# Kernel tuning notes

Hardware: AMD Instinct MI355X
Metric: run time of the kernel (lower is better)

Reference implementation:

```python
import jax, jax.numpy as jnp
import numpy as np

T = 3072          # num tokens
HID = 5120        # hidden_size
H = 16            # num_local_heads
DN = 128          # qk_nope_head_dim
DR = 64           # qk_rope_head_dim
DQK = DN + DR     # qk_head_dim = 192
DV = 128          # v_head_dim
Q_RANK = 1536     # q_lora_rank
KV_RANK = 512     # kv_lora_rank


def rmsnorm(x, w, eps=1e-6):
    var = jnp.mean(jnp.square(x), axis=-1, keepdims=True)
    return x * jax.lax.rsqrt(var + eps) * w


def apply_rope(x, cos, sin):
    # neox-style rotate-half; x [..., DR], cos/sin broadcastable [..., DR//2]
    x1, x2 = jnp.split(x, 2, axis=-1)
    return jnp.concatenate([x1 * cos - x2 * sin, x2 * cos + x1 * sin], axis=-1)


def setup_inputs() -> dict:
    key = jax.random.key(0)
    ks = jax.random.split(key, 8)
    s = 0.02
    positions = jnp.arange(T, dtype=jnp.int32)
    hidden_states = jax.random.normal(ks[0], (T, HID), dtype=jnp.float32)
    llama_4_scaling = jnp.ones((T, 1, 1), dtype=jnp.float32)
    w_q_a = jax.random.normal(ks[1], (HID, Q_RANK), dtype=jnp.float32) * s
    q_a_ln_w = jnp.ones((Q_RANK,), dtype=jnp.float32)
    w_q_b = jax.random.normal(ks[2], (Q_RANK, H * DQK), dtype=jnp.float32) * s
    w_kv_a = jax.random.normal(ks[3], (HID, KV_RANK + DR), dtype=jnp.float32) * s
    kv_a_ln_w = jnp.ones((KV_RANK,), dtype=jnp.float32)
    w_kv_b = jax.random.normal(ks[4], (KV_RANK, H * (DN + DV)), dtype=jnp.float32) * s
    w_o = jax.random.normal(ks[5], (H * DV, HID), dtype=jnp.float32) * s
    # cos/sin cache: [max_pos, DR]; first half cos, second half sin
    inv_freq = 1.0 / (10000.0 ** (jnp.arange(0, DR, 2, dtype=jnp.float32) / DR))
    t = jnp.arange(T, dtype=jnp.float32)
    freqs = t[:, None] * inv_freq[None, :]              # [T, DR//2]
    cos_sin_cache = jnp.concatenate([jnp.cos(freqs), jnp.sin(freqs)], axis=-1)
    return {
        "positions": positions, "hidden_states": hidden_states,
        "llama_4_scaling": llama_4_scaling,
        "w_q_a": w_q_a, "q_a_ln_w": q_a_ln_w, "w_q_b": w_q_b,
        "w_kv_a": w_kv_a, "kv_a_ln_w": kv_a_ln_w, "w_kv_b": w_kv_b,
        "w_o": w_o, "cos_sin_cache": cos_sin_cache,
    }


def reference(positions, hidden_states, llama_4_scaling, w_q_a, q_a_ln_w,
              w_q_b, w_kv_a, kv_a_ln_w, w_kv_b, w_o, cos_sin_cache):
    # ---- Q path: low-rank down/up projection with RMSNorm ----
    q = rmsnorm(hidden_states @ w_q_a, q_a_ln_w) @ w_q_b       # [T, H*DQK]
    q = q.reshape(T, H, DQK)
    q_nope, q_pe = q[..., :DN], q[..., DN:]                    # [T,H,DN],[T,H,DR]

    # ---- KV path: compressed latent + shared rope key ----
    latent = hidden_states @ w_kv_a                            # [T, KV_RANK+DR]
    kv_a = rmsnorm(latent[:, :KV_RANK], kv_a_ln_w)             # [T, KV_RANK]
    k_pe = latent[:, KV_RANK:]                                 # [T, DR] (shared across heads)
    kv = (kv_a @ w_kv_b).reshape(T, H, DN + DV)
    k_nope, v = kv[..., :DN], kv[..., DN:]                     # [T,H,DN],[T,H,DV]

    # ---- partial RoPE on the rope slices only ----
    cs = cos_sin_cache[positions]                              # [T, DR]
    cos, sin = cs[:, :DR // 2], cs[:, DR // 2:]
    q_pe = apply_rope(q_pe, cos[:, None, :], sin[:, None, :])
    k_pe = apply_rope(k_pe, cos, sin)

    q = jnp.concatenate([q_nope, q_pe], axis=-1)               # [T, H, DQK]
    k = jnp.concatenate(
        [k_nope, jnp.broadcast_to(k_pe[:, None, :], (T, H, DR))], axis=-1)

    q = q * llama_4_scaling

    # ---- causal attention (v is zero-padded to DQK in the original;
    #      the pad contributes zeros and is sliced off, so we skip it) ----
    scale = 1.0 / jnp.sqrt(jnp.float32(DQK))
    scores = jnp.einsum('qhd,khd->hqk', q, k) * scale          # [H, T, T]
    causal = positions[:, None] >= positions[None, :]
    scores = jnp.where(causal[None, :, :], scores, jnp.finfo(scores.dtype).min)
    probs = jax.nn.softmax(scores, axis=-1)
    attn = jnp.einsum('hqk,khd->qhd', probs, v)                # [T, H, DV]

    return attn.reshape(T, H * DV) @ w_o                       # [T, HID]
```

## Files before the change

kernel.cpp:

```cpp
#include <hip/hip_runtime.h>
#include <hip/hip_bf16.h>
#include <math.h>

#define T_TOK 3072
#define HID_D 5120
#define NH 16
#define DN 128
#define DR 64
#define DQK 192
#define DV 128
#define QRANK 1536
#define KVRANK 512
#define MERGED_N 2176

typedef __attribute__((ext_vector_type(8))) short short8;
typedef __attribute__((ext_vector_type(4))) float f32x4;
typedef unsigned short u16;

__device__ __forceinline__ u16 f2bf(float f) {
    unsigned int u = __float_as_uint(f);
    unsigned int lsb = (u >> 16) & 1;
    u += 0x7fffu + lsb;
    return (u16)(u >> 16);
}
__device__ __forceinline__ float bf2f(u16 v) {
    return __uint_as_float(((unsigned int)v) << 16);
}

__device__ __forceinline__ void gload_lds16(const u16* g, u16* l) {
    __builtin_amdgcn_global_load_lds((const __attribute__((address_space(1))) void*)g,
                                     (__attribute__((address_space(3))) void*)l, 16, 0, 0);
}

__global__ __launch_bounds__(256) void convert_bf_k(const float* __restrict__ x,
                                                    u16* __restrict__ y, int n4)
{
    const int i = blockIdx.x * 256 + threadIdx.x;
    if (i < n4) {
        float4 v = ((const float4*)x)[i];
        ushort4 o;
        o.x = f2bf(v.x); o.y = f2bf(v.y); o.z = f2bf(v.z); o.w = f2bf(v.w);
        ((ushort4*)y)[i] = o;
    }
}

__global__ __launch_bounds__(256) void transpose_conv_k(const float* __restrict__ W,
                                                        u16* __restrict__ WT,
                                                        int K, int N)
{
    __shared__ float tile[32][33];
    const int n0 = blockIdx.x * 32, k0 = blockIdx.y * 32;
    const int tx = threadIdx.x & 31, ty = threadIdx.x >> 5;
#pragma unroll
    for (int i = 0; i < 32; i += 8) {
        const int nn = n0 + tx;
        tile[ty + i][tx] = (nn < N) ? W[(size_t)(k0 + ty + i) * N + nn] : 0.f;
    }
    __syncthreads();
#pragma unroll
    for (int i = 0; i < 32; i += 8) {
        WT[(size_t)(n0 + ty + i) * K + k0 + tx] = f2bf(tile[tx][ty + i]);
    }
}

template <bool BF16_OUT>
__global__ __launch_bounds__(256) void bgemm_bt_k(
    const u16* __restrict__ A, const u16* __restrict__ BT, void* __restrict__ C,
    int Nreal, int K, int lda, int ldb, int ldc)
{
    __shared__ __attribute__((aligned(16))) u16 As[128 * 32];
    __shared__ __attribute__((aligned(16))) u16 Bs[128 * 32];

    const int tid  = threadIdx.x;
    const int wave = tid >> 6, lane = tid & 63;
    const int quad = lane >> 4, l16 = lane & 15;
    const int wr = (wave >> 1) * 64, wc = (wave & 1) * 64;
    const int row0 = blockIdx.y * 128, col0 = blockIdx.x * 128;

    f32x4 acc[4][4];
#pragma unroll
    for (int i = 0; i < 4; ++i)
#pragma unroll
        for (int j = 0; j < 4; ++j) acc[i][j] = (f32x4){0.f, 0.f, 0.f, 0.f};

    const int sr  = tid >> 2;
    const int skc = (tid & 3) * 8;
    const u16* ap0 = A  + (size_t)(row0 + sr)      * lda + skc;
    const u16* ap1 = A  + (size_t)(row0 + sr + 64) * lda + skc;
    const u16* bp0 = BT + (size_t)(col0 + sr)      * ldb + skc;
    const u16* bp1 = BT + (size_t)(col0 + sr + 64) * ldb + skc;
    u16* al0 = As + tid * 8;
    u16* al1 = As + tid * 8 + 64 * 32;
    u16* bl0 = Bs + tid * 8;
    u16* bl1 = Bs + tid * 8 + 64 * 32;

    for (int kt = 0; kt < K; kt += 32) {
        gload_lds16(ap0 + kt, al0);
        gload_lds16(ap1 + kt, al1);
        gload_lds16(bp0 + kt, bl0);
        gload_lds16(bp1 + kt, bl1);
        __syncthreads();

        short8 af[4], bf[4];
#pragma unroll
        for (int mi = 0; mi < 4; ++mi)
            af[mi] = *(const short8*)(As + (wr + mi * 16 + l16) * 32 + quad * 8);
#pragma unroll
        for (int ni = 0; ni < 4; ++ni)
            bf[ni] = *(const short8*)(Bs + (wc + ni * 16 + l16) * 32 + quad * 8);
#pragma unroll
        for (int mi = 0; mi < 4; ++mi)
#pragma unroll
            for (int ni = 0; ni < 4; ++ni)
                acc[mi][ni] = __builtin_amdgcn_mfma_f32_16x16x32_bf16(
                    af[mi], bf[ni], acc[mi][ni], 0, 0, 0);
        __syncthreads();
    }

#pragma unroll
    for (int mi = 0; mi < 4; ++mi) {
#pragma unroll
        for (int ni = 0; ni < 4; ++ni) {
            const int col_g = col0 + wc + ni * 16 + l16;
            if (col_g < Nreal) {
#pragma unroll
                for (int r = 0; r < 4; ++r) {
                    const int row_g = row0 + wr + mi * 16 + quad * 4 + r;
                    if (BF16_OUT)
                        ((u16*)C)[(size_t)row_g * ldc + col_g] = f2bf(acc[mi][ni][r]);
                    else
                        ((float*)C)[(size_t)row_g * ldc + col_g] = acc[mi][ni][r];
                }
            }
        }
    }
}

__global__ __launch_bounds__(256) void rmsnorm_bf_k(const u16* __restrict__ x,
                                                    const float* __restrict__ w,
                                                    u16* __restrict__ y,
                                                    int width, int stride, int off)
{
    const int row = blockIdx.x;
    const u16* xr = x + (size_t)row * stride + off;
    const int nch = width >> 3;
    float ss = 0.f;
    for (int i = threadIdx.x; i < nch; i += 256) {
        short8 v = *(const short8*)(xr + i * 8);
#pragma unroll
        for (int j = 0; j < 8; ++j) { const float f = bf2f((u16)v[j]); ss += f * f; }
    }
    __shared__ float red[256];
    red[threadIdx.x] = ss;
    __syncthreads();
    for (int s2 = 128; s2 > 0; s2 >>= 1) {
        if (threadIdx.x < s2) red[threadIdx.x] += red[threadIdx.x + s2];
        __syncthreads();
    }
    const float scale = rsqrtf(red[0] / (float)width + 1e-6f);
    u16* yr = y + (size_t)row * width;
    for (int i = threadIdx.x; i < nch; i += 256) {
        short8 v = *(const short8*)(xr + i * 8);
        const float4 w0 = *(const float4*)(w + i * 8);
        const float4 w1 = *(const float4*)(w + i * 8 + 4);
        short8 o;
        o[0] = (short)f2bf(bf2f((u16)v[0]) * scale * w0.x);
        o[1] = (short)f2bf(bf2f((u16)v[1]) * scale * w0.y);
        o[2] = (short)f2bf(bf2f((u16)v[2]) * scale * w0.z);
        o[3] = (short)f2bf(bf2f((u16)v[3]) * scale * w0.w);
        o[4] = (short)f2bf(bf2f((u16)v[4]) * scale * w1.x);
        o[5] = (short)f2bf(bf2f((u16)v[5]) * scale * w1.y);
        o[6] = (short)f2bf(bf2f((u16)v[6]) * scale * w1.z);
        o[7] = (short)f2bf(bf2f((u16)v[7]) * scale * w1.w);
        *(short8*)(yr + i * 8) = o;
    }
}

__global__ __launch_bounds__(256) void rope_scale_q_bf_k(const u16* __restrict__ q, const int* __restrict__ positions,
                                  const float* __restrict__ scaling,
                                  const float* __restrict__ cs_cache, u16* __restrict__ qb)
{
    const int t = blockIdx.x;
    const int pos = positions[t];
    const float* cs = cs_cache + (size_t)pos * DR;
    const float s = scaling[t];
    __shared__ float c_sh[32], s_sh[32];
    if (threadIdx.x < 32) {
        c_sh[threadIdx.x] = cs[threadIdx.x];
        s_sh[threadIdx.x] = cs[32 + threadIdx.x];
    }
    __syncthreads();
    const u16* qt = q + (size_t)t * NH * DQK;
    u16* qo = qb + (size_t)t * NH * DQK;
    for (int cc = threadIdx.x; cc < NH * 20; cc += 256) {
        const int hh = cc / 20, c = cc % 20;
        const u16* qr = qt + hh * DQK;
        u16* qw = qo + hh * DQK;
        if (c < 16) {
            short8 v = *(const short8*)(qr + c * 8);
            short8 o;
#pragma unroll
            for (int j = 0; j < 8; ++j) o[j] = (short)f2bf(bf2f((u16)v[j]) * s);
            *(short8*)(qw + c * 8) = o;
        } else {
            const int d0 = (c - 16) * 8;
            short8 x1 = *(const short8*)(qr + 128 + d0);
            short8 x2 = *(const short8*)(qr + 160 + d0);
            short8 o1, o2;
#pragma unroll
            for (int j = 0; j < 8; ++j) {
                const float a = bf2f((u16)x1[j]), b = bf2f((u16)x2[j]);
                const float cv = c_sh[d0 + j], sv = s_sh[d0 + j];
                o1[j] = (short)f2bf((a * cv - b * sv) * s);
                o2[j] = (short)f2bf((b * cv + a * sv) * s);
            }
            *(short8*)(qw + 128 + d0) = o1;
            *(short8*)(qw + 160 + d0) = o2;
        }
    }
}

__global__ void rope_k_bf_k(const u16* __restrict__ qa_lat, u16* __restrict__ kpe,
                            const int* __restrict__ positions,
                            const float* __restrict__ cs_cache)
{
    const int t = blockIdx.x;
    const int d = threadIdx.x;
    if (d >= 32) return;
    const int pos = positions[t];
    const float* cs = cs_cache + (size_t)pos * DR;
    const float c = cs[d], sn = cs[32 + d];
    const u16* lr = qa_lat + (size_t)t * MERGED_N + QRANK + KVRANK;
    const float x1 = bf2f(lr[d]), x2 = bf2f(lr[32 + d]);
    kpe[(size_t)t * DR + d]      = f2bf(x1 * c - x2 * sn);
    kpe[(size_t)t * DR + 32 + d] = f2bf(x2 * c + x1 * sn);
}

__global__ __launch_bounds__(256) void transpose_v_k(const u16* __restrict__ kvb,
                                                     u16* __restrict__ vt)
{
    __shared__ u16 tile[64][72];
    const int t0 = blockIdx.x * 64, d0 = blockIdx.y * 64, h = blockIdx.z;
    const int tid = threadIdx.x;
    for (int cc = tid; cc < 64 * 8; cc += 256) {
        const int row = cc >> 3, c = (cc & 7) * 8;
        *(short8*)&tile[row][c] =
            *(const short8*)(kvb + ((size_t)(t0 + row) * NH + h) * (DN + DV) + DN + d0 + c);
    }
    __syncthreads();
    for (int cc = tid; cc < 64 * 8; cc += 256) {
        const int drow = cc >> 3, c = (cc & 7) * 8;
        short8 s;
#pragma unroll
        for (int j = 0; j < 8; ++j) s[j] = tile[c + j][drow];
        *(short8*)(vt + ((size_t)h * DV + d0 + drow) * T_TOK + t0 + c) = s;
    }
}

#define ATT_BM 128
#define ATT_BN 64
__global__ __launch_bounds__(512, 4) void attn_mfma_k(
    const u16* __restrict__ qb, const u16* __restrict__ kvb,
    const u16* __restrict__ kpeb, const u16* __restrict__ vt,
    u16* __restrict__ attnb)
{
    __shared__ u16 Ks[ATT_BN][200];
    __shared__ u16 Vt[DV][72];
    __shared__ u16 Ps[8][16][72];

    const int tid  = threadIdx.x;
    const int wave = tid >> 6;
    const int lane = tid & 63;
    const int quad = lane >> 4;
    const int l16  = lane & 15;

    const int bid   = (int)blockIdx.x;
    const int chunk = bid & 7;
    const int local = bid >> 3;
    const int h     = chunk * 2 + (local & 1);
    const int qblk  = (T_TOK / ATT_BM - 1) - (local >> 1);
    const int q0    = qblk * ATT_BM;
    const int wrow0 = q0 + wave * 16;
    const int qrow  = wrow0 + l16;

    short8 qf[6];
    {
        const u16* qp = qb + ((size_t)qrow * NH + h) * DQK + quad * 8;
#pragma unroll
        for (int c = 0; c < 6; ++c)
            qf[c] = *(const short8*)(qp + c * 32);
    }

    const u16* gp[5];
    size_t     gst[5];
    u16*       ld[5];
#pragma unroll
    for (int i = 0; i < 3; ++i) {
        const int cc = tid + 512 * i;
        const int row = cc / 24, c = cc % 24;
        if (c < 16) {
            gp[i]  = kvb + ((size_t)row * NH + h) * (DN + DV) + c * 8;
            gst[i] = (size_t)ATT_BN * NH * (DN + DV);
        } else {
            gp[i]  = kpeb + (size_t)row * DR + (c - 16) * 8;
            gst[i] = (size_t)ATT_BN * DR;
        }
        ld[i] = &Ks[row][c * 8];
    }
#pragma unroll
    for (int i = 0; i < 2; ++i) {
        const int cc = tid + 512 * i;
        const int row = cc >> 3, c = (cc & 7) * 8;
        gp[3 + i]  = vt + ((size_t)h * DV + row) * T_TOK + c;
        gst[3 + i] = (size_t)ATT_BN;
        ld[3 + i]  = &Vt[row][c];
    }

    f32x4 oacc[8];
#pragma unroll
    for (int t = 0; t < 8; ++t) oacc[t] = (f32x4){0.f, 0.f, 0.f, 0.f};
    float m_old[4], l_run[4];
#pragma unroll
    for (int r = 0; r < 4; ++r) { m_old[r] = -1e30f; l_run[r] = 0.f; }

    short8 streg[5];
#pragma unroll
    for (int i = 0; i < 5; ++i) streg[i] = *(const short8*)gp[i];

    const int nkt = (q0 + ATT_BM) / ATT_BN;
    for (int kt = 0; kt < nkt; ++kt) {
        __syncthreads();
#pragma unroll
        for (int i = 0; i < 5; ++i) *(short8*)ld[i] = streg[i];
        __syncthreads();
        if (kt + 1 < nkt) {
#pragma unroll
            for (int i = 0; i < 5; ++i)
                streg[i] = *(const short8*)(gp[i] + (size_t)(kt + 1) * gst[i]);
        }

        const int k0 = kt * ATT_BN;
        if (k0 <= wrow0 + 15) {
            f32x4 sacc[4];
#pragma unroll
            for (int t = 0; t < 4; ++t) sacc[t] = (f32x4){0.f, 0.f, 0.f, 0.f};
#pragma unroll
            for (int t = 0; t < 4; ++t) {
                const u16* kp = &Ks[t * 16 + l16][quad * 8];
#pragma unroll
                for (int c = 0; c < 6; ++c) {
                    short8 bfrag = *(const short8*)(kp + c * 32);
                    sacc[t] = __builtin_amdgcn_mfma_f32_16x16x32_bf16(qf[c], bfrag, sacc[t], 0, 0, 0);
                }
            }
            const float sc = 0.07216878364870322f;
            const int rbase = wrow0 + quad * 4;
            if (k0 + ATT_BN - 1 > wrow0) {
#pragma unroll
                for (int t = 0; t < 4; ++t) {
                    const int colg = k0 + t * 16 + l16;
#pragma unroll
                    for (int r = 0; r < 4; ++r) {
                        const float s = sacc[t][r] * sc;
                        sacc[t][r] = (rbase + r >= colg) ? s : -1e30f;
                    }
                }
            } else {
#pragma unroll
                for (int t = 0; t < 4; ++t)
#pragma unroll
                    for (int r = 0; r < 4; ++r) sacc[t][r] *= sc;
            }
            float alpha[4];
#pragma unroll
            for (int r = 0; r < 4; ++r) {
                float mx = fmaxf(fmaxf(sacc[0][r], sacc[1][r]), fmaxf(sacc[2][r], sacc[3][r]));
                mx = fmaxf(mx, __shfl_xor(mx, 1));
                mx = fmaxf(mx, __shfl_xor(mx, 2));
                mx = fmaxf(mx, __shfl_xor(mx, 4));
                mx = fmaxf(mx, __shfl_xor(mx, 8));
                const float mnew = fmaxf(m_old[r], mx);
                alpha[r] = __expf(m_old[r] - mnew);
                float sum = 0.f;
#pragma unroll
                for (int t = 0; t < 4; ++t) {
                    const float p = __expf(sacc[t][r] - mnew);
                    sacc[t][r] = p;
                    sum += p;
                }
                sum += __shfl_xor(sum, 1);
                sum += __shfl_xor(sum, 2);
                sum += __shfl_xor(sum, 4);
                sum += __shfl_xor(sum, 8);
                l_run[r] = l_run[r] * alpha[r] + sum;
                m_old[r] = mnew;
            }
#pragma unroll
            for (int t = 0; t < 4; ++t)
#pragma unroll
                for (int r = 0; r < 4; ++r)
                    Ps[wave][quad * 4 + r][t * 16 + l16] = f2bf(sacc[t][r]);
#pragma unroll
            for (int t = 0; t < 8; ++t)
#pragma unroll
                for (int r = 0; r < 4; ++r)
                    oacc[t][r] *= alpha[r];
#pragma unroll
            for (int ch = 0; ch < 2; ++ch) {
                short8 pfrag = *(const short8*)&Ps[wave][l16][ch * 32 + quad * 8];
#pragma unroll
                for (int t = 0; t < 8; ++t) {
                    short8 vfrag = *(const short8*)&Vt[t * 16 + l16][ch * 32 + quad * 8];
                    oacc[t] = __builtin_amdgcn_mfma_f32_16x16x32_bf16(pfrag, vfrag, oacc[t], 0, 0, 0);
                }
            }
        }
    }

#pragma unroll
    for (int r = 0; r < 4; ++r) {
        const float linv = 1.f / l_run[r];
        const int row_g = wrow0 + quad * 4 + r;
        u16* op = attnb + (size_t)row_g * (NH * DV) + h * DV;
#pragma unroll
        for (int t = 0; t < 8; ++t)
            op[t * 16 + l16] = f2bf(oacc[t][r] * linv);
    }
}

extern "C" void kernel_launch(void* const* d_in, const int* in_sizes, int n_in,
                              void* d_out, int out_size, void* d_ws, size_t ws_size,
                              hipStream_t stream)
{
    const int*   positions = (const int*)d_in[0];
    const float* hidden    = (const float*)d_in[1];
    const float* scaling   = (const float*)d_in[2];
    const float* w_q_a     = (const float*)d_in[3];
    const float* q_a_ln_w  = (const float*)d_in[4];
    const float* w_q_b     = (const float*)d_in[5];
    const float* w_kv_a    = (const float*)d_in[6];
    const float* kv_a_ln_w = (const float*)d_in[7];
    const float* w_kv_b    = (const float*)d_in[8];
    const float* w_o       = (const float*)d_in[9];
    const float* cs_cache  = (const float*)d_in[10];
    float* out = (float*)d_out;

    char* p = (char*)d_ws;
    auto alloc = [&](size_t bytes) { char* r = p; p += (bytes + 255) & ~(size_t)255; return r; };

    char* regH      = alloc((size_t)T_TOK * HID_D * 2);
    u16*  hidden_bf = (u16*)regH;
    u16*  qraw_bf   = (u16*)regH;
    char* regQ      = alloc((size_t)T_TOK * MERGED_N * 2 + (size_t)T_TOK * QRANK * 2);
    u16*  qa_lat    = (u16*)regQ;
    u16*  q_a_norm  = (u16*)(regQ + (size_t)T_TOK * MERGED_N * 2);
    u16*  qb        = (u16*)regQ;
    u16* kv_a_norm = (u16*)alloc((size_t)T_TOK * KVRANK * 2);
    u16* kpe_bf    = (u16*)alloc((size_t)T_TOK * DR * 2);
    u16* kv_bf     = (u16*)alloc((size_t)T_TOK * NH * (DN + DV) * 2);
    u16* vt        = (u16*)alloc((size_t)NH * DV * T_TOK * 2);
    u16* attnb     = (u16*)alloc((size_t)T_TOK * NH * DV * 2);
    u16* wqakva_bt = (u16*)alloc((size_t)MERGED_N * HID_D * 2);
    u16* wqb_bt    = (u16*)alloc((size_t)(NH * DQK) * QRANK * 2);
    u16* wkvb_bt   = (u16*)alloc((size_t)(NH * (DN + DV)) * KVRANK * 2);
    u16* wo_bt     = (u16*)alloc((size_t)HID_D * (NH * DV) * 2);

    const dim3 blk(256);

    convert_bf_k<<<dim3((T_TOK * HID_D / 4 + 255) / 256), blk, 0, stream>>>(
        hidden, hidden_bf, T_TOK * HID_D / 4);
    transpose_conv_k<<<dim3(QRANK / 32, HID_D / 32), blk, 0, stream>>>(
        w_q_a, wqakva_bt, HID_D, QRANK);
    transpose_conv_k<<<dim3(640 / 32, HID_D / 32), blk, 0, stream>>>(
        w_kv_a, wqakva_bt + (size_t)QRANK * HID_D, HID_D, KVRANK + DR);
    transpose_conv_k<<<dim3(NH * DQK / 32, QRANK / 32), blk, 0, stream>>>(w_q_b, wqb_bt, QRANK, NH * DQK);
    transpose_conv_k<<<dim3(NH * (DN + DV) / 32, KVRANK / 32), blk, 0, stream>>>(w_kv_b, wkvb_bt, KVRANK, NH * (DN + DV));
    transpose_conv_k<<<dim3(HID_D / 32, NH * DV / 32), blk, 0, stream>>>(w_o, wo_bt, NH * DV, HID_D);

    bgemm_bt_k<true><<<dim3(MERGED_N / 128, T_TOK / 128), blk, 0, stream>>>(
        hidden_bf, wqakva_bt, qa_lat, QRANK + KVRANK + DR, HID_D, HID_D, HID_D, MERGED_N);
    rope_k_bf_k<<<dim3(T_TOK), dim3(64), 0, stream>>>(qa_lat, kpe_bf, positions, cs_cache);
    rmsnorm_bf_k<<<dim3(T_TOK), blk, 0, stream>>>(qa_lat, q_a_ln_w, q_a_norm, QRANK, MERGED_N, 0);
    rmsnorm_bf_k<<<dim3(T_TOK), blk, 0, stream>>>(qa_lat, kv_a_ln_w, kv_a_norm, KVRANK, MERGED_N, QRANK);
    bgemm_bt_k<true><<<dim3(NH * DQK / 128, T_TOK / 128), blk, 0, stream>>>(
        q_a_norm, wqb_bt, qraw_bf, NH * DQK, QRANK, QRANK, QRANK, NH * DQK);
    rope_scale_q_bf_k<<<dim3(T_TOK), blk, 0, stream>>>(qraw_bf, positions, scaling, cs_cache, qb);
    bgemm_bt_k<true><<<dim3(NH * (DN + DV) / 128, T_TOK / 128), blk, 0, stream>>>(
        kv_a_norm, wkvb_bt, kv_bf, NH * (DN + DV), KVRANK, KVRANK, KVRANK, NH * (DN + DV));
    transpose_v_k<<<dim3(T_TOK / 64, DV / 64, NH), blk, 0, stream>>>(kv_bf, vt);
    attn_mfma_k<<<dim3(T_TOK / ATT_BM * NH), dim3(512), 0, stream>>>(qb, kv_bf, kpe_bf, vt, attnb);
    bgemm_bt_k<false><<<dim3(HID_D / 128, T_TOK / 128), blk, 0, stream>>>(
        attnb, wo_bt, out, HID_D, NH * DV, NH * DV, NH * DV, HID_D);
}
```

Measured before the change: 838.3 us.

## Load K and V fragments directly from global memory in attention, dropping LDS staging

The attention kernel no longer stages K/K_pe and transposed V tiles through shared memory with register prefetch and block barriers. Each wave now reads its MFMA B-operand fragments straight from global memory, with no __syncthreads in the key loop. Blocks shrink to 256 threads (4 waves, 64 query rows), the grid becomes 768 blocks, and each wave iterates only up to its own causal limit. This removes barrier and LDS traffic, but each wave reloads K/V independently, which increases global/L2 traffic and exposes load latency without explicit prefetch.

```diff
diff --git a/kernel.cpp b/kernel.cpp
--- a/kernel.cpp
+++ b/kernel.cpp
@@ -257,16 +257,12 @@
     }
 }
 
-#define ATT_BM 128
-#define ATT_BN 64
-__global__ __launch_bounds__(512, 4) void attn_mfma_k(
+__global__ __launch_bounds__(256) void attn_mfma_k(
     const u16* __restrict__ qb, const u16* __restrict__ kvb,
     const u16* __restrict__ kpeb, const u16* __restrict__ vt,
     u16* __restrict__ attnb)
 {
-    __shared__ u16 Ks[ATT_BN][200];
-    __shared__ u16 Vt[DV][72];
-    __shared__ u16 Ps[8][16][72];
+    __shared__ u16 Ps[4][16][72];
 
     const int tid  = threadIdx.x;
     const int wave = tid >> 6;
@@ -278,9 +274,8 @@
     const int chunk = bid & 7;
     const int local = bid >> 3;
     const int h     = chunk * 2 + (local & 1);
-    const int qblk  = (T_TOK / ATT_BM - 1) - (local >> 1);
-    const int q0    = qblk * ATT_BM;
-    const int wrow0 = q0 + wave * 16;
+    const int qb64  = 47 - (local >> 1);
+    const int wrow0 = qb64 * 64 + wave * 16;
     const int qrow  = wrow0 + l16;
 
     short8 qf[6];
@@ -291,31 +286,6 @@
             qf[c] = *(const short8*)(qp + c * 32);
     }
 
-    const u16* gp[5];
-    size_t     gst[5];
-    u16*       ld[5];
-#pragma unroll
-    for (int i = 0; i < 3; ++i) {
-        const int cc = tid + 512 * i;
-        const int row = cc / 24, c = cc % 24;
-        if (c < 16) {
-            gp[i]  = kvb + ((size_t)row * NH + h) * (DN + DV) + c * 8;
-            gst[i] = (size_t)ATT_BN * NH * (DN + DV);
-        } else {
-            gp[i]  = kpeb + (size_t)row * DR + (c - 16) * 8;
-            gst[i] = (size_t)ATT_BN * DR;
-        }
-        ld[i] = &Ks[row][c * 8];
-    }
-#pragma unroll
-    for (int i = 0; i < 2; ++i) {
-        const int cc = tid + 512 * i;
-        const int row = cc >> 3, c = (cc & 7) * 8;
-        gp[3 + i]  = vt + ((size_t)h * DV + row) * T_TOK + c;
-        gst[3 + i] = (size_t)ATT_BN;
-        ld[3 + i]  = &Vt[row][c];
-    }
-
     f32x4 oacc[8];
 #pragma unroll
     for (int t = 0; t < 8; ++t) oacc[t] = (f32x4){0.f, 0.f, 0.f, 0.f};
@@ -323,96 +293,91 @@
 #pragma unroll
     for (int r = 0; r < 4; ++r) { m_old[r] = -1e30f; l_run[r] = 0.f; }
 
-    short8 streg[5];
-#pragma unroll
-    for (int i = 0; i < 5; ++i) streg[i] = *(const short8*)gp[i];
-
-    const int nkt = (q0 + ATT_BM) / ATT_BN;
+    const u16* vbase = vt + ((size_t)h * DV + l16) * T_TOK + quad * 8;
+    const int nkt = wrow0 / 64 + 1;
+
     for (int kt = 0; kt < nkt; ++kt) {
-        __syncthreads();
-#pragma unroll
-        for (int i = 0; i < 5; ++i) *(short8*)ld[i] = streg[i];
-        __syncthreads();
-        if (kt + 1 < nkt) {
-#pragma unroll
-            for (int i = 0; i < 5; ++i)
-                streg[i] = *(const short8*)(gp[i] + (size_t)(kt + 1) * gst[i]);
-        }
-
-        const int k0 = kt * ATT_BN;
-        if (k0 <= wrow0 + 15) {
-            f32x4 sacc[4];
-#pragma unroll
-            for (int t = 0; t < 4; ++t) sacc[t] = (f32x4){0.f, 0.f, 0.f, 0.f};
+        const int k0 = kt * 64;
+        f32x4 sacc[4];
+#pragma unroll
+        for (int t = 0; t < 4; ++t) sacc[t] = (f32x4){0.f, 0.f, 0.f, 0.f};
+#pragma unroll
+        for (int t = 0; t < 4; ++t) {
+            const int krow = k0 + t * 16 + l16;
+            const u16* kr = kvb + ((size_t)krow * NH + h) * (DN + DV) + quad * 8;
+            const u16* pr = kpeb + (size_t)krow * DR + quad * 8;
+            short8 b0 = *(const short8*)(kr);
+            short8 b1 = *(const short8*)(kr + 32);
+            short8 b2 = *(const short8*)(kr + 64);
+            short8 b3 = *(const short8*)(kr + 96);
+            short8 b4 = *(const short8*)(pr);
+            short8 b5 = *(const short8*)(pr + 32);
+            sacc[t] = __builtin_amdgcn_mfma_f32_16x16x32_bf16(qf[0], b0, sacc[t], 0, 0, 0);
+            sacc[t] = __builtin_amdgcn_mfma_f32_16x16x32_bf16(qf[1], b1, sacc[t], 0, 0, 0);
+            sacc[t] = __builtin_amdgcn_mfma_f32_16x16x32_bf16(qf[2], b2, sacc[t], 0, 0, 0);
+            sacc[t] = __builtin_amdgcn_mfma_f32_16x16x32_bf16(qf[3], b3, sacc[t], 0, 0, 0);
+            sacc[t] = __builtin_amdgcn_mfma_f32_16x16x32_bf16(qf[4], b4, sacc[t], 0, 0, 0);
+            sacc[t] = __builtin_amdgcn_mfma_f32_16x16x32_bf16(qf[5], b5, sacc[t], 0, 0, 0);
+        }
+        const float sc = 0.07216878364870322f;
+        const int rbase = wrow0 + quad * 4;
+        if (kt == nkt - 1) {
 #pragma unroll
             for (int t = 0; t < 4; ++t) {
-                const u16* kp = &Ks[t * 16 + l16][quad * 8];
-#pragma unroll
-                for (int c = 0; c < 6; ++c) {
-                    short8 bfrag = *(const short8*)(kp + c * 32);
-                    sacc[t] = __builtin_amdgcn_mfma_f32_16x16x32_bf16(qf[c], bfrag, sacc[t], 0, 0, 0);
+                const int colg = k0 + t * 16 + l16;
+#pragma unroll
+                for (int r = 0; r < 4; ++r) {
+                    const float s = sacc[t][r] * sc;
+                    sacc[t][r] = (rbase + r >= colg) ? s : -1e30f;
                 }
             }
-            const float sc = 0.07216878364870322f;
-            const int rbase = wrow0 + quad * 4;
-            if (k0 + ATT_BN - 1 > wrow0) {
-#pragma unroll
-                for (int t = 0; t < 4; ++t) {
-                    const int colg = k0 + t * 16 + l16;
-#pragma unroll
-                    for (int r = 0; r < 4; ++r) {
-                        const float s = sacc[t][r] * sc;
-                        sacc[t][r] = (rbase + r >= colg) ? s : -1e30f;
-                    }
-                }
-            } else {
-#pragma unroll
-                for (int t = 0; t < 4; ++t)
-#pragma unroll
-                    for (int r = 0; r < 4; ++r) sacc[t][r] *= sc;
+        } else {
+#pragma unroll
+            for (int t = 0; t < 4; ++t)
+#pragma unroll
+                for (int r = 0; r < 4; ++r) sacc[t][r] *= sc;
+        }
+        float alpha[4];
+#pragma unroll
+        for (int r = 0; r < 4; ++r) {
+            float mx = fmaxf(fmaxf(sacc[0][r], sacc[1][r]), fmaxf(sacc[2][r], sacc[3][r]));
+            mx = fmaxf(mx, __shfl_xor(mx, 1));
+            mx = fmaxf(mx, __shfl_xor(mx, 2));
+            mx = fmaxf(mx, __shfl_xor(mx, 4));
+            mx = fmaxf(mx, __shfl_xor(mx, 8));
+            const float mnew = fmaxf(m_old[r], mx);
+            alpha[r] = __expf(m_old[r] - mnew);
+            float sum = 0.f;
+#pragma unroll
+            for (int t = 0; t < 4; ++t) {
+                const float p = __expf(sacc[t][r] - mnew);
+                sacc[t][r] = p;
+                sum += p;
             }
-            float alpha[4];
-#pragma unroll
-            for (int r = 0; r < 4; ++r) {
-                float mx = fmaxf(fmaxf(sacc[0][r], sacc[1][r]), fmaxf(sacc[2][r], sacc[3][r]));
-                mx = fmaxf(mx, __shfl_xor(mx, 1));
-                mx = fmaxf(mx, __shfl_xor(mx, 2));
-                mx = fmaxf(mx, __shfl_xor(mx, 4));
-                mx = fmaxf(mx, __shfl_xor(mx, 8));
-                const float mnew = fmaxf(m_old[r], mx);
-                alpha[r] = __expf(m_old[r] - mnew);
-                float sum = 0.f;
-#pragma unroll
-                for (int t = 0; t < 4; ++t) {
-                    const float p = __expf(sacc[t][r] - mnew);
-                    sacc[t][r] = p;
-                    sum += p;
-                }
-                sum += __shfl_xor(sum, 1);
-                sum += __shfl_xor(sum, 2);
-                sum += __shfl_xor(sum, 4);
-                sum += __shfl_xor(sum, 8);
-                l_run[r] = l_run[r] * alpha[r] + sum;
-                m_old[r] = mnew;
-            }
-#pragma unroll
-            for (int t = 0; t < 4; ++t)
-#pragma unroll
-                for (int r = 0; r < 4; ++r)
-                    Ps[wave][quad * 4 + r][t * 16 + l16] = f2bf(sacc[t][r]);
-#pragma unroll
-            for (int t = 0; t < 8; ++t)
-#pragma unroll
-                for (int r = 0; r < 4; ++r)
-                    oacc[t][r] *= alpha[r];
-#pragma unroll
-            for (int ch = 0; ch < 2; ++ch) {
-                short8 pfrag = *(const short8*)&Ps[wave][l16][ch * 32 + quad * 8];
-#pragma unroll
-                for (int t = 0; t < 8; ++t) {
-                    short8 vfrag = *(const short8*)&Vt[t * 16 + l16][ch * 32 + quad * 8];
-                    oacc[t] = __builtin_amdgcn_mfma_f32_16x16x32_bf16(pfrag, vfrag, oacc[t], 0, 0, 0);
-                }
+            sum += __shfl_xor(sum, 1);
+            sum += __shfl_xor(sum, 2);
+            sum += __shfl_xor(sum, 4);
+            sum += __shfl_xor(sum, 8);
+            l_run[r] = l_run[r] * alpha[r] + sum;
+            m_old[r] = mnew;
+        }
+#pragma unroll
+        for (int t = 0; t < 4; ++t)
+#pragma unroll
+            for (int r = 0; r < 4; ++r)
+                Ps[wave][quad * 4 + r][t * 16 + l16] = f2bf(sacc[t][r]);
+#pragma unroll
+        for (int t = 0; t < 8; ++t)
+#pragma unroll
+            for (int r = 0; r < 4; ++r)
+                oacc[t][r] *= alpha[r];
+#pragma unroll
+        for (int ch = 0; ch < 2; ++ch) {
+            short8 pfrag = *(const short8*)&Ps[wave][l16][ch * 32 + quad * 8];
+#pragma unroll
+            for (int t = 0; t < 8; ++t) {
+                short8 vfrag = *(const short8*)(vbase + (size_t)t * 16 * T_TOK + k0 + ch * 32);
+                oacc[t] = __builtin_amdgcn_mfma_f32_16x16x32_bf16(pfrag, vfrag, oacc[t], 0, 0, 0);
             }
         }
     }
@@ -488,7 +453,7 @@
     bgemm_bt_k<true><<<dim3(NH * (DN + DV) / 128, T_TOK / 128), blk, 0, stream>>>(
         kv_a_norm, wkvb_bt, kv_bf, NH * (DN + DV), KVRANK, KVRANK, KVRANK, NH * (DN + DV));
     transpose_v_k<<<dim3(T_TOK / 64, DV / 64, NH), blk, 0, stream>>>(kv_bf, vt);
-    attn_mfma_k<<<dim3(T_TOK / ATT_BM * NH), dim3(512), 0, stream>>>(qb, kv_bf, kpe_bf, vt, attnb);
+    attn_mfma_k<<<dim3(768), dim3(256), 0, stream>>>(qb, kv_bf, kpe_bf, vt, attnb);
     bgemm_bt_k<false><<<dim3(HID_D / 128, T_TOK / 128), blk, 0, stream>>>(
         attnb, wo_bt, out, HID_D, NH * DV, NH * DV, NH * DV, HID_D);
 }
```

Measured after the change: 992.8 us. 18.4% more time.
